# Kernel tuning notes

Measured on AMD Instinct MI355X. Metric: run time of the kernel, lower is better.

## Reference

```python
import jax, jax.numpy as jnp
import numpy as np

R = 40000      # aug_num_rels
E = 500000     # number of relation-graph triplets
DIN = 64       # rel_emb_dim
DH = 64        # hid_dim_rel
H = 8          # num_head
DHID = DH // H # 8
NBIN = 10
L = 2          # num_layer_rel


def _leaky(x):
    return jax.nn.leaky_relu(x, negative_slope=0.2)


def _rel_layer(emb_rel, head, tail, binidx, pw, pb, abin, avec, aw, ab):
    # emb_rel: [R, DH]; head/tail/binidx: [E]
    concat = jnp.concatenate([emb_rel[head], emb_rel[tail]], axis=-1)  # [E, 2*DH]
    z = _leaky(concat @ pw + pb).reshape(-1, H, DHID)                   # [E, H, DHID]
    # attention logits: per-head dot with attn_vec + leaky(bin bias)
    raw = (z * avec[None]).sum(-1) + _leaky(abin[binidx, :, 0])         # [E, H]
    # segmented softmax over edges grouped by head index
    m = jax.ops.segment_max(raw, head, num_segments=R)                  # [R, H]
    e = jnp.exp(raw - m[head])                                          # [E, H]
    s = jax.ops.segment_sum(e, head, num_segments=R)                    # [R, H]
    beta = e / (s[head] + 1e-16)                                        # [E, H]
    msg = (emb_rel[tail] @ aw + ab).reshape(-1, H, DHID) * beta[..., None]
    out = jax.ops.segment_sum(msg, head, num_segments=R)                # [R, H, DHID]
    return out.reshape(R, DH)


def setup_inputs() -> dict:
    key = jax.random.key(0)
    ks = jax.random.split(key, 12)
    ht = jax.random.randint(ks[0], (E, 2), 0, R)
    b = jax.random.randint(ks[1], (E, 1), 0, NBIN)
    relation_triplets = jnp.concatenate([ht, b], axis=-1).astype(jnp.int64)
    sc = 0.05
    return {
        "relation_triplets": relation_triplets,
        "rel_emb_w": jax.random.normal(ks[2], (R, DIN), jnp.float32) * sc,
        "proj1_w": jax.random.normal(ks[3], (DIN, DH), jnp.float32) * sc,
        "proj1_b": jnp.zeros((DH,), jnp.float32),
        "attn_proj_w": jax.random.normal(ks[4], (L, 2 * DH, DH), jnp.float32) * sc,
        "attn_proj_b": jnp.zeros((L, DH), jnp.float32),
        "attn_bin": jax.random.normal(ks[5], (L, NBIN, H, 1), jnp.float32) * sc,
        "attn_vec": jax.random.normal(ks[6], (L, H, DHID), jnp.float32) * sc,
        "aggr_w": jax.random.normal(ks[7], (L, DH, DH), jnp.float32) * sc,
        "aggr_b": jnp.zeros((L, DH), jnp.float32),
        "res_w": jax.random.normal(ks[8], (L, DH, DH), jnp.float32) * sc,
        "res_b": jnp.zeros((L, DH), jnp.float32),
    }


def reference(relation_triplets, rel_emb_w, proj1_w, proj1_b, attn_proj_w,
              attn_proj_b, attn_bin, attn_vec, aggr_w, aggr_b, res_w, res_b):
    head = relation_triplets[:, 0]
    tail = relation_triplets[:, 1]
    binidx = relation_triplets[:, 2]
    emb_rel = jax.nn.relu(rel_emb_w @ proj1_w + proj1_b)  # [R, DH]
    for l in range(L):
        h = _rel_layer(emb_rel, head, tail, binidx,
                       attn_proj_w[l], attn_proj_b[l], attn_bin[l],
                       attn_vec[l], aggr_w[l], aggr_b[l])
        h = jax.nn.relu(h)
        emb_rel = h + jax.nn.relu(emb_rel @ res_w[l] + res_b[l])
    return emb_rel
```

## Files before the change

kernel.cpp:

```cpp
#include <hip/hip_runtime.h>
#include <hip/hip_bf16.h>

typedef __hip_bfloat16 bf16;

#define R_NUM 40000
#define E_NUM 500000

#define W_P1W 0
#define W_P1B 4096
#define W_APW 4160
#define W_APB 20544
#define W_ABIN 20672
#define W_AVEC 20832
#define W_AW 20960
#define W_AB 29152
#define W_RW 29280
#define W_RB 37472
#define W_END 37600
#define WCONV_BLOCKS 147

#define O_FLAG 0
#define O_WBUF 256
#define O_ROWP 150784
#define O_CNTS 310784
#define O_TMP 470784
#define O_PART 634624
#define O_STB 635136
#define O_BIG 2635392
#define XMP_BYTES 10240000ull
#define HR_BYTES 20480000ull
#define XM32_BYTES 20480000ull
#define NEED_LEAN (O_BIG + XMP_BYTES + HR_BYTES)
#define NEED_XM1 (O_BIG + XM32_BYTES)

static __device__ __forceinline__ float b2f(bf16 x) { return __bfloat162float(x); }
static __device__ __forceinline__ float ldv(const float* p, size_t i) { return p[i]; }
static __device__ __forceinline__ float ldv(const bf16* p, size_t i) { return __bfloat162float(p[i]); }
static __device__ __forceinline__ void stv(float* p, size_t i, float v) { p[i] = v; }
static __device__ __forceinline__ void stv(bf16* p, size_t i, float v) { p[i] = __float2bfloat16(v); }

static __device__ __forceinline__ unsigned int f2bb(float x) {
  union { float f; unsigned int u; } v;
  v.f = x;
  unsigned int r = v.u + 0x7FFFu + ((v.u >> 16) & 1u);
  return r >> 16;
}
static __device__ __forceinline__ unsigned int packxm(float xt, float mt) {
  return f2bb(xt) | (f2bb(mt) << 16);
}


__global__ void k_detect_init(const unsigned int* __restrict__ trip_w,
                              const unsigned short* __restrict__ emb_w, int* __restrict__ flag,
                              int* __restrict__ counts, int* __restrict__ stb) {
  int tid = threadIdx.x;
  if (blockIdx.x == 0) {
    if (tid < 64) {
      int lane = tid;
      unsigned int acc = 0;
      for (int i = lane; i < 1024; i += 64) acc |= trip_w[2 * i + 1];
      int votes = 0;
      for (int i = lane; i < 2048; i += 64) {
        unsigned short u = emb_w[2 * i];
        int ex = (u >> 7) & 0xFF;
        if (ex >= 90 && ex <= 130) votes++;
      }
      for (int off = 1; off < 64; off <<= 1) {
        acc |= __shfl_xor(acc, off);
        votes += __shfl_xor(votes, off);
      }
      if (lane == 0) {
        flag[0] = (acc == 0) ? 1 : 0;
        flag[1] = (votes < 1024) ? 1 : 0;
      }
    }
    return;
  }
  int g = (blockIdx.x - 1) * 256 + tid;
  for (int i = g; i < R_NUM; i += 159 * 256) counts[i] = 0;
  if (blockIdx.x == 1 && tid < 64) stb[E_NUM + tid] = 0;
}


static __device__ __forceinline__ void load_edge(const unsigned int* __restrict__ w, int e,
                                                 int i64, int& h, int& t, int& b) {
  if (i64) {
    h = (int)w[6 * e + 0];
    t = (int)w[6 * e + 2];
    b = (int)w[6 * e + 4];
  } else {
    h = (int)w[3 * e + 0];
    t = (int)w[3 * e + 1];
    b = (int)w[3 * e + 2];
  }
}

__global__ void k_hist_wconv(const unsigned int* __restrict__ trip_w, const int* __restrict__ flag,
                             int* __restrict__ counts, const void* p1w, const void* p1b,
                             const void* apw, const void* apb, const void* abin, const void* avec,
                             const void* aw, const void* ab, const void* rw, const void* rb,
                             float* __restrict__ wbuf) {
  if (blockIdx.x < WCONV_BLOCKS) {
    int i = blockIdx.x * 256 + threadIdx.x;
    if (i >= W_END) return;
    const void* src;
    int off;
    if (i < W_P1B) { src = p1w; off = i - W_P1W; }
    else if (i < W_APW) { src = p1b; off = i - W_P1B; }
    else if (i < W_APB) { src = apw; off = i - W_APW; }
    else if (i < W_ABIN) { src = apb; off = i - W_APB; }
    else if (i < W_AVEC) { src = abin; off = i - W_ABIN; }
    else if (i < W_AW) { src = avec; off = i - W_AVEC; }
    else if (i < W_AB) { src = aw; off = i - W_AW; }
    else if (i < W_RW) { src = ab; off = i - W_AB; }
    else if (i < W_RB) { src = rw; off = i - W_RW; }
    else { src = rb; off = i - W_RB; }
    wbuf[i] = flag[1] ? ((const float*)src)[off] : b2f(((const bf16*)src)[off]);
    return;
  }
  int e = (blockIdx.x - WCONV_BLOCKS) * 256 + threadIdx.x;
  if (e >= E_NUM) return;
  int h, t, b;
  load_edge(trip_w, e, flag[0], h, t, b);
  atomicAdd(&counts[h], 1);
}


__global__ void k_scan_a(const int* __restrict__ counts, int* __restrict__ tmp,
                         int* __restrict__ partial) {
  __shared__ int sd[1024];
  int tid = threadIdx.x;
  int idx = blockIdx.x * 1024 + tid;
  int v = (idx < R_NUM) ? counts[idx] : 0;
  sd[tid] = v;
  __syncthreads();
  for (int off = 1; off < 1024; off <<= 1) {
    int t = (tid >= off) ? sd[tid - off] : 0;
    __syncthreads();
    sd[tid] += t;
    __syncthreads();
  }
  if (idx < R_NUM) tmp[idx] = sd[tid];
  if (tid == 1023) partial[blockIdx.x] = sd[1023];
}

__global__ void k_scan_c(const int* __restrict__ counts, const int* __restrict__ tmp,
                         const int* __restrict__ partial, int* __restrict__ row_ptr) {
  __shared__ int soff;
  if (threadIdx.x < 64) {
    int lane = threadIdx.x;
    int p = (lane < (int)blockIdx.x) ? partial[lane] : 0;
    for (int d = 1; d < 64; d <<= 1) p += __shfl_xor(p, d);
    if (lane == 0) soff = p;
  }
  __syncthreads();
  int idx = blockIdx.x * 1024 + threadIdx.x;
  if (idx < R_NUM) row_ptr[idx] = tmp[idx] - counts[idx] + soff;
}

__global__ void k_scatter(const unsigned int* __restrict__ trip_w, const int* __restrict__ flag,
                          int* __restrict__ row_ptr, int* __restrict__ stb) {
  int e = blockIdx.x * 256 + threadIdx.x;
  if (e >= E_NUM) return;
  int h, t, b;
  load_edge(trip_w, e, flag[0], h, t, b);
  int pos = atomicAdd(&row_ptr[h], 1);
  stb[pos] = (t & 0xFFFF) | (b << 16);
}


__global__ void __launch_bounds__(256, 4) k_emb0xm_p(const void* __restrict__ A,
                                                     const int* __restrict__ flag,
                                                     const float* __restrict__ wbuf,
                                                     float* __restrict__ emb,
                                                     unsigned int* __restrict__ XMp,
                                                     float2* __restrict__ HR) {
  int j = threadIdx.x & 63;
  int g = threadIdx.x >> 6;
  int r0 = blockIdx.x * 32 + g * 8;
  int f32 = flag[1];
  __shared__ float sA[32][64];
  for (int k = threadIdx.x; k < 2048; k += 256) {
    int rr = k >> 6, cc = k & 63;
    size_t idx = (size_t)(blockIdx.x * 32 + rr) * 64 + cc;
    sA[rr][cc] = f32 ? ((const float*)A)[idx] : b2f(((const bf16*)A)[idx]);
  }
  __syncthreads();
  int base = g * 8;
  float a[8] = {0.f, 0.f, 0.f, 0.f, 0.f, 0.f, 0.f, 0.f};
  {
    const float* W = wbuf + W_P1W;
    for (int i4 = 0; i4 < 64; i4 += 4) {
      float4 ev[8];
#pragma unroll
      for (int n = 0; n < 8; n++) ev[n] = *(const float4*)&sA[base + n][i4];
#pragma unroll
      for (int di = 0; di < 4; di++) {
        float w = W[(i4 + di) * 64 + j];
#pragma unroll
        for (int n = 0; n < 8; n++)
          a[n] = fmaf(((const float*)&ev[n])[di], w, a[n]);
      }
    }
    float bj = wbuf[W_P1B + j];
#pragma unroll
    for (int n = 0; n < 8; n++) {
      a[n] = fmaxf(a[n] + bj, 0.f);
      emb[(size_t)(r0 + n) * 64 + j] = a[n];
    }
  }
  __syncthreads();
#pragma unroll
  for (int n = 0; n < 8; n++) sA[base + n][j] = a[n];
  __syncthreads();
  {
    const float* pwb = wbuf + W_APW + 4096;
    const float* aw = wbuf + W_AW;
    const float* pwt = wbuf + W_APW;
    const float* rw = wbuf + W_RW;
    float axt[8] = {0.f, 0.f, 0.f, 0.f, 0.f, 0.f, 0.f, 0.f};
    float amt[8] = {0.f, 0.f, 0.f, 0.f, 0.f, 0.f, 0.f, 0.f};
    float axh[8] = {0.f, 0.f, 0.f, 0.f, 0.f, 0.f, 0.f, 0.f};
    float ars[8] = {0.f, 0.f, 0.f, 0.f, 0.f, 0.f, 0.f, 0.f};
    for (int i4 = 0; i4 < 64; i4 += 4) {
      float4 ev[8];
#pragma unroll
      for (int n = 0; n < 8; n++) ev[n] = *(const float4*)&sA[base + n][i4];
#pragma unroll
      for (int di = 0; di < 4; di++) {
        int i = i4 + di;
        float wt = pwb[i * 64 + j];
        float wm = aw[i * 64 + j];
        float wh = pwt[i * 64 + j];
        float wr = rw[i * 64 + j];
#pragma unroll
        for (int n = 0; n < 8; n++) {
          float e = ((const float*)&ev[n])[di];
          axt[n] = fmaf(e, wt, axt[n]);
          amt[n] = fmaf(e, wm, amt[n]);
          axh[n] = fmaf(e, wh, axh[n]);
          ars[n] = fmaf(e, wr, ars[n]);
        }
      }
    }
    float abj = wbuf[W_AB + j];
    float pbj = wbuf[W_APB + j];
    float rbj = wbuf[W_RB + j];
#pragma unroll
    for (int n = 0; n < 8; n++) {
      XMp[(size_t)(r0 + n) * 64 + j] = packxm(axt[n], amt[n] + abj);
      HR[(size_t)(r0 + n) * 64 + j] = make_float2(axh[n] + pbj, fmaxf(ars[n] + rbj, 0.f));
    }
  }
}


__global__ void __launch_bounds__(256, 4) k_xmhr_p(const float* __restrict__ emb,
                                                   const float* __restrict__ wbuf, int l,
                                                   unsigned int* __restrict__ XMp,
                                                   float2* __restrict__ HR) {
  int j = threadIdx.x & 63;
  int g = threadIdx.x >> 6;
  int r0 = blockIdx.x * 32 + g * 8;
  __shared__ float sE[32][64];
  for (int k = threadIdx.x; k < 2048; k += 256) {
    int rr = k >> 6, cc = k & 63;
    sE[rr][cc] = emb[(size_t)(blockIdx.x * 32 + rr) * 64 + cc];
  }
  __syncthreads();
  int base = g * 8;
  const float* pwb = wbuf + W_APW + l * 8192 + 4096;
  const float* aw = wbuf + W_AW + l * 4096;
  const float* pwt = wbuf + W_APW + l * 8192;
  const float* rw = wbuf + W_RW + l * 4096;
  float axt[8] = {0.f, 0.f, 0.f, 0.f, 0.f, 0.f, 0.f, 0.f};
  float amt[8] = {0.f, 0.f, 0.f, 0.f, 0.f, 0.f, 0.f, 0.f};
  float axh[8] = {0.f, 0.f, 0.f, 0.f, 0.f, 0.f, 0.f, 0.f};
  float ars[8] = {0.f, 0.f, 0.f, 0.f, 0.f, 0.f, 0.f, 0.f};
  for (int i4 = 0; i4 < 64; i4 += 4) {
    float4 ev[8];
#pragma unroll
    for (int n = 0; n < 8; n++) ev[n] = *(const float4*)&sE[base + n][i4];
#pragma unroll
    for (int di = 0; di < 4; di++) {
      int i = i4 + di;
      float wt = pwb[i * 64 + j];
      float wm = aw[i * 64 + j];
      float wh = pwt[i * 64 + j];
      float wr = rw[i * 64 + j];
#pragma unroll
      for (int n = 0; n < 8; n++) {
        float e = ((const float*)&ev[n])[di];
        axt[n] = fmaf(e, wt, axt[n]);
        amt[n] = fmaf(e, wm, amt[n]);
        axh[n] = fmaf(e, wh, axh[n]);
        ars[n] = fmaf(e, wr, ars[n]);
      }
    }
  }
  float abj = wbuf[W_AB + l * 64 + j];
  float pbj = wbuf[W_APB + l * 64 + j];
  float rbj = wbuf[W_RB + l * 64 + j];
#pragma unroll
  for (int n = 0; n < 8; n++) {
    XMp[(size_t)(r0 + n) * 64 + j] = packxm(axt[n], amt[n] + abj);
    HR[(size_t)(r0 + n) * 64 + j] = make_float2(axh[n] + pbj, fmaxf(ars[n] + rbj, 0.f));
  }
}


__global__ void __launch_bounds__(256, 4) k_edge_lean(
    const int* __restrict__ row_ptr, const int* __restrict__ stb,
    const unsigned int* __restrict__ XMp, const float2* __restrict__ HR,
    const float* __restrict__ wbuf, int l, float* __restrict__ emb) {
  __shared__ float sab[80];
  int tid = threadIdx.x;
  int lane = tid & 63;
  int w = tid >> 6;
  int hh = lane >> 3;
  if (tid < 80) {
    float a = wbuf[W_ABIN + l * 80 + tid];
    sab[tid] = (a > 0.f) ? a : 0.2f * a;
  }
  __syncthreads();
  float av = wbuf[W_AVEC + l * 64 + lane];

  int r = blockIdx.x * 4 + w;
  float2 hr = HR[(size_t)r * 64 + lane];
  int beg = (r == 0) ? 0 : row_ptr[r - 1];
  int end = row_ptr[r];
  beg = __builtin_amdgcn_readfirstlane(beg);
  end = __builtin_amdgcn_readfirstlane(end);

  float xh = hr.x;
  float num = 0.f, den = 0.f;
  for (int j = beg; j < end; j += 16) {
    int pk[16];
    unsigned int xp[16];
#pragma unroll
    for (int k = 0; k < 16; k++) pk[k] = stb[j + k];
#pragma unroll
    for (int k = 0; k < 16; k++)
      xp[k] = XMp[(size_t)(pk[k] & 0xFFFF) * 64 + lane];
#pragma unroll
    for (int k = 0; k < 16; k++) {
      float xt = __uint_as_float(xp[k] << 16);
      float mt = __uint_as_float(xp[k] & 0xFFFF0000u);
      float z = xh + xt;
      z = (z > 0.f) ? z : 0.2f * z;
      float v = z * av;
      v += __shfl_xor(v, 1);
      v += __shfl_xor(v, 2);
      v += __shfl_xor(v, 4);
      float e = __expf(v + sab[(pk[k] >> 16) * 8 + hh]);
      e = (j + k < end) ? e : 0.f;
      den += e;
      num = fmaf(mt, e, num);
    }
  }
  emb[(size_t)r * 64 + lane] = fmaxf(num / (den + 1e-16f), 0.f) + hr.y;
}


__global__ void k_emb0(const void* __restrict__ A, const int* __restrict__ flag,
                       const float* __restrict__ wbuf, float* __restrict__ emb) {
  int j = threadIdx.x & 63;
  int g = threadIdx.x >> 6;
  int r0 = blockIdx.x * 16 + g * 4;
  int f32 = flag[1];
  __shared__ float sA[16][64];
  for (int k = threadIdx.x; k < 1024; k += 256) {
    int rr = k >> 6, cc = k & 63;
    size_t idx = (size_t)(blockIdx.x * 16 + rr) * 64 + cc;
    sA[rr][cc] = f32 ? ((const float*)A)[idx] : b2f(((const bf16*)A)[idx]);
  }
  __syncthreads();
  const float* W = wbuf + W_P1W;
  float a[4] = {0.f, 0.f, 0.f, 0.f};
  int base = g * 4;
  for (int i = 0; i < 64; i++) {
    float w = W[i * 64 + j];
#pragma unroll
    for (int n = 0; n < 4; n++) a[n] = fmaf(sA[base + n][i], w, a[n]);
  }
  float bj = wbuf[W_P1B + j];
#pragma unroll
  for (int n = 0; n < 4; n++)
    emb[(size_t)(r0 + n) * 64 + j] = fmaxf(a[n] + bj, 0.f);
}

__global__ void k_xm(const float* __restrict__ emb, const float* __restrict__ wbuf, int l,
                     float2* __restrict__ XM) {
  int j = threadIdx.x & 63;
  int g = threadIdx.x >> 6;
  int r0 = blockIdx.x * 16 + g * 4;
  __shared__ float sE[16][64];
  for (int k = threadIdx.x; k < 1024; k += 256) {
    int rr = k >> 6, cc = k & 63;
    sE[rr][cc] = emb[(size_t)(blockIdx.x * 16 + rr) * 64 + cc];
  }
  __syncthreads();
  const float* pwb = wbuf + W_APW + l * 8192 + 4096;
  const float* aw = wbuf + W_AW + l * 4096;
  float axt[4] = {0.f, 0.f, 0.f, 0.f};
  float amt[4] = {0.f, 0.f, 0.f, 0.f};
  int base = g * 4;
  for (int i = 0; i < 64; i++) {
    float wt = pwb[i * 64 + j];
    float wm = aw[i * 64 + j];
#pragma unroll
    for (int n = 0; n < 4; n++) {
      float e = sE[base + n][i];
      axt[n] = fmaf(e, wt, axt[n]);
      amt[n] = fmaf(e, wm, amt[n]);
    }
  }
  float abj = wbuf[W_AB + l * 64 + j];
#pragma unroll
  for (int n = 0; n < 4; n++)
    XM[(size_t)(r0 + n) * 64 + j] = make_float2(axt[n], amt[n] + abj);
}

__global__ void __launch_bounds__(256, 4) k_edge_f(
    const int* __restrict__ row_ptr, const int* __restrict__ stb, const float2* __restrict__ XM,
    const float* __restrict__ wbuf, int l, float* __restrict__ emb) {
  __shared__ float sab[80];
  int tid = threadIdx.x;
  int lane = tid & 63;
  int w = tid >> 6;
  int hh = lane >> 3;
  if (tid < 80) {
    float a = wbuf[W_ABIN + l * 80 + tid];
    sab[tid] = (a > 0.f) ? a : 0.2f * a;
  }
  __syncthreads();

  const float* pwt = wbuf + W_APW + l * 8192;
  const float* rwp = wbuf + W_RW + l * 4096;
  float av = wbuf[W_AVEC + l * 64 + lane];
  float xh0 = wbuf[W_APB + l * 64 + lane];
  float res0 = wbuf[W_RB + l * 64 + lane];

  int r0 = blockIdx.x * 16 + w * 4;
  for (int rr = 0; rr < 4; rr++) {
    int r = r0 + rr;
    float ev = emb[(size_t)r * 64 + lane];
    float xh = xh0, res = res0;
#pragma unroll 16
    for (int i = 0; i < 64; i++) {
      float e = __shfl(ev, i);
      xh = fmaf(e, pwt[i * 64 + lane], xh);
      res = fmaf(e, rwp[i * 64 + lane], res);
    }
    res = fmaxf(res, 0.f);

    int beg = (r == 0) ? 0 : row_ptr[r - 1];
    int end = row_ptr[r];
    beg = __builtin_amdgcn_readfirstlane(beg);
    end = __builtin_amdgcn_readfirstlane(end);

    float num = 0.f, den = 0.f;
    for (int j = beg; j < end; j += 16) {
      int pk[16];
      float2 xmv[16];
#pragma unroll
      for (int k = 0; k < 16; k++) pk[k] = stb[j + k];
#pragma unroll
      for (int k = 0; k < 16; k++) xmv[k] = XM[(size_t)(pk[k] & 0xFFFF) * 64 + lane];
#pragma unroll
      for (int k = 0; k < 16; k++) {
        float z = xh + xmv[k].x;
        z = (z > 0.f) ? z : 0.2f * z;
        float v = z * av;
        v += __shfl_xor(v, 1);
        v += __shfl_xor(v, 2);
        v += __shfl_xor(v, 4);
        float e = __expf(v + sab[(pk[k] >> 16) * 8 + hh]);
        e = (j + k < end) ? e : 0.f;
        den += e;
        num = fmaf(xmv[k].y, e, num);
      }
    }
    emb[(size_t)r * 64 + lane] = fmaxf(num / (den + 1e-16f), 0.f) + res;
  }
}


static __device__ __forceinline__ float dotcol(const float* __restrict__ Wm, float val, int lane) {
  float acc = 0.f;
  for (int i = 0; i < 64; i++) acc = fmaf(__shfl(val, i), Wm[i * 64 + lane], acc);
  return acc;
}

template <typename TIN, typename TOUT>
__global__ void k_edge_d(const int* __restrict__ row_ptr, const int* __restrict__ stb,
                         const float* __restrict__ wbuf, int l, const TIN* __restrict__ emb_in,
                         TOUT* __restrict__ emb_out) {
  __shared__ float sab[80];
  int tid = threadIdx.x;
  int lane = tid & 63;
  int w = tid >> 6;
  int r = blockIdx.x * 4 + w;
  int hh = lane >> 3;
  if (tid < 80) {
    float a = wbuf[W_ABIN + l * 80 + tid];
    sab[tid] = (a > 0.f) ? a : 0.2f * a;
  }
  __syncthreads();
  const float* pwt = wbuf + W_APW + l * 8192;
  const float* pwb = pwt + 4096;
  const float* aw = wbuf + W_AW + l * 4096;
  const float* rw = wbuf + W_RW + l * 4096;

  float ev = ldv(emb_in, (size_t)r * 64 + lane);
  float xh = wbuf[W_APB + l * 64 + lane];
  float res = wbuf[W_RB + l * 64 + lane];
  for (int i = 0; i < 64; i++) {
    float e = __shfl(ev, i);
    xh = fmaf(e, pwt[i * 64 + lane], xh);
    res = fmaf(e, rw[i * 64 + lane], res);
  }
  res = fmaxf(res, 0.f);
  float av = wbuf[W_AVEC + l * 64 + lane];
  float abl = wbuf[W_AB + l * 64 + lane];

  int beg = (r == 0) ? 0 : row_ptr[r - 1];
  int end = row_ptr[r];
  float num = 0.f, den = 0.f;
  for (int j = beg; j < end; j++) {
    int p = stb[j];
    int t = p & 0xFFFF;
    float tv = ldv(emb_in, (size_t)t * 64 + lane);
    float z = xh + dotcol(pwb, tv, lane);
    z = (z > 0.f) ? z : 0.2f * z;
    float v = z * av;
    v += __shfl_xor(v, 1);
    v += __shfl_xor(v, 2);
    v += __shfl_xor(v, 4);
    float e = __expf(v + sab[(p >> 16) * 8 + hh]);
    den += e;
    float mt = dotcol(aw, tv, lane) + abl;
    num = fmaf(mt, e, num);
  }
  stv(emb_out, (size_t)r * 64 + lane, fmaxf(num / (den + 1e-16f), 0.f) + res);
}


extern "C" void kernel_launch(void* const* d_in, const int* in_sizes, int n_in,
                              void* d_out, int out_size, void* d_ws, size_t ws_size,
                              hipStream_t stream) {
  const unsigned int* trip_w = (const unsigned int*)d_in[0];
  const void* rel_emb = d_in[1];
  float* emb = (float*)d_out;

  char* ws = (char*)d_ws;
  int* flag = (int*)(ws + O_FLAG);
  float* wbuf = (float*)(ws + O_WBUF);
  int* row_ptr = (int*)(ws + O_ROWP);
  int* counts = (int*)(ws + O_CNTS);
  int* tmp = (int*)(ws + O_TMP);
  int* partial = (int*)(ws + O_PART);
  int* stb = (int*)(ws + O_STB);
  char* big = ws + O_BIG;

  k_detect_init<<<160, 256, 0, stream>>>(trip_w, (const unsigned short*)rel_emb, flag, counts,
                                         stb);
  int eb_blocks = (E_NUM + 255) / 256;
  k_hist_wconv<<<WCONV_BLOCKS + eb_blocks, 256, 0, stream>>>(
      trip_w, flag, counts, d_in[2], d_in[3], d_in[4], d_in[5], d_in[6], d_in[7], d_in[8],
      d_in[9], d_in[10], d_in[11], wbuf);
  k_scan_a<<<40, 1024, 0, stream>>>(counts, tmp, partial);
  k_scan_c<<<40, 1024, 0, stream>>>(counts, tmp, partial, row_ptr);
  k_scatter<<<eb_blocks, 256, 0, stream>>>(trip_w, flag, row_ptr, stb);

  if (ws_size >= NEED_LEAN) {
    unsigned int* XMp = (unsigned int*)big;
    float2* HR = (float2*)(big + XMP_BYTES);
    k_emb0xm_p<<<R_NUM / 32, 256, 0, stream>>>(rel_emb, flag, wbuf, emb, XMp, HR);
    k_edge_lean<<<R_NUM / 4, 256, 0, stream>>>(row_ptr, stb, XMp, HR, wbuf, 0, emb);
    k_xmhr_p<<<R_NUM / 32, 256, 0, stream>>>(emb, wbuf, 1, XMp, HR);
    k_edge_lean<<<R_NUM / 4, 256, 0, stream>>>(row_ptr, stb, XMp, HR, wbuf, 1, emb);
  } else if (ws_size >= NEED_XM1) {
    float2* XM = (float2*)big;
    k_emb0<<<R_NUM / 16, 256, 0, stream>>>(rel_emb, flag, wbuf, emb);
    k_xm<<<R_NUM / 16, 256, 0, stream>>>(emb, wbuf, 0, XM);
    k_edge_f<<<R_NUM / 16, 256, 0, stream>>>(row_ptr, stb, XM, wbuf, 0, emb);
    k_xm<<<R_NUM / 16, 256, 0, stream>>>(emb, wbuf, 1, XM);
    k_edge_f<<<R_NUM / 16, 256, 0, stream>>>(row_ptr, stb, XM, wbuf, 1, emb);
  } else {
    k_emb0<<<R_NUM / 16, 256, 0, stream>>>(rel_emb, flag, wbuf, emb);
    bf16* embB = (bf16*)big;
    k_edge_d<float, bf16><<<R_NUM / 4, 256, 0, stream>>>(row_ptr, stb, wbuf, 0, emb, embB);
    k_edge_d<bf16, float><<<R_NUM / 4, 256, 0, stream>>>(row_ptr, stb, wbuf, 1, embB, emb);
  }
}
```

Before: 258.4 us.

## Fuse histogram with layer-0 transforms and layer-1 transforms into edge kernel

Result: slower. 267.5 us (+3.5%).

```diff
diff --git a/kernel.cpp b/kernel.cpp
--- a/kernel.cpp
+++ b/kernel.cpp
@@ -5,6 +5,17 @@
 
 #define R_NUM 40000
 #define E_NUM 500000
+#define HIST_BLOCKS 1954
+#define XF_BLOCKS 1250
+
+#define N_CNTS 0
+#define N_ROWP 160000
+#define N_STB 320000
+#define N_XMP0 2320384
+#define N_HR0 12560384
+#define N_XMP1 33040384
+#define N_HR1 43280384
+#define NEED2 63760384ull
 
 #define W_P1W 0
 #define W_P1B 4096
@@ -27,11 +38,6 @@
 #define O_PART 634624
 #define O_STB 635136
 #define O_BIG 2635392
-#define XMP_BYTES 10240000ull
-#define HR_BYTES 20480000ull
-#define XM32_BYTES 20480000ull
-#define NEED_LEAN (O_BIG + XMP_BYTES + HR_BYTES)
-#define NEED_XM1 (O_BIG + XM32_BYTES)
 
 static __device__ __forceinline__ float b2f(bf16 x) { return __bfloat162float(x); }
 static __device__ __forceinline__ float ldv(const float* p, size_t i) { return p[i]; }
@@ -47,6 +53,19 @@
 }
 static __device__ __forceinline__ unsigned int packxm(float xt, float mt) {
   return f2bb(xt) | (f2bb(mt) << 16);
+}
+
+static __device__ __forceinline__ void load_edge(const unsigned int* __restrict__ w, int e,
+                                                 int i64, int& h, int& t, int& b) {
+  if (i64) {
+    h = (int)w[6 * e + 0];
+    t = (int)w[6 * e + 2];
+    b = (int)w[6 * e + 4];
+  } else {
+    h = (int)w[3 * e + 0];
+    t = (int)w[3 * e + 1];
+    b = (int)w[3 * e + 2];
+  }
 }
 
 
@@ -82,18 +101,316 @@
 }
 
 
-static __device__ __forceinline__ void load_edge(const unsigned int* __restrict__ w, int e,
-                                                 int i64, int& h, int& t, int& b) {
-  if (i64) {
-    h = (int)w[6 * e + 0];
-    t = (int)w[6 * e + 2];
-    b = (int)w[6 * e + 4];
-  } else {
-    h = (int)w[3 * e + 0];
-    t = (int)w[3 * e + 1];
-    b = (int)w[3 * e + 2];
-  }
-}
+template <typename WT>
+static __device__ __forceinline__ void xf4t(const float (*sA)[64], int base, int j, int l,
+                                            const WT* __restrict__ apw, const WT* __restrict__ apb,
+                                            const WT* __restrict__ aw, const WT* __restrict__ ab,
+                                            const WT* __restrict__ rw, const WT* __restrict__ rb,
+                                            int r0, unsigned int* __restrict__ XMp,
+                                            float2* __restrict__ HR) {
+  const WT* pwt = apw + l * 8192;
+  const WT* pwb = pwt + 4096;
+  const WT* awl = aw + l * 4096;
+  const WT* rwl = rw + l * 4096;
+  float axt[8] = {0.f, 0.f, 0.f, 0.f, 0.f, 0.f, 0.f, 0.f};
+  float amt[8] = {0.f, 0.f, 0.f, 0.f, 0.f, 0.f, 0.f, 0.f};
+  float axh[8] = {0.f, 0.f, 0.f, 0.f, 0.f, 0.f, 0.f, 0.f};
+  float ars[8] = {0.f, 0.f, 0.f, 0.f, 0.f, 0.f, 0.f, 0.f};
+  for (int i4 = 0; i4 < 64; i4 += 4) {
+    float4 ev[8];
+#pragma unroll
+    for (int n = 0; n < 8; n++) ev[n] = *(const float4*)&sA[base + n][i4];
+#pragma unroll
+    for (int di = 0; di < 4; di++) {
+      int i = i4 + di;
+      float wt = ldv(pwb, (size_t)i * 64 + j);
+      float wm = ldv(awl, (size_t)i * 64 + j);
+      float wh = ldv(pwt, (size_t)i * 64 + j);
+      float wr = ldv(rwl, (size_t)i * 64 + j);
+#pragma unroll
+      for (int n = 0; n < 8; n++) {
+        float e = ((const float*)&ev[n])[di];
+        axt[n] = fmaf(e, wt, axt[n]);
+        amt[n] = fmaf(e, wm, amt[n]);
+        axh[n] = fmaf(e, wh, axh[n]);
+        ars[n] = fmaf(e, wr, ars[n]);
+      }
+    }
+  }
+  float abj = ldv(ab, (size_t)l * 64 + j);
+  float pbj = ldv(apb, (size_t)l * 64 + j);
+  float rbj = ldv(rb, (size_t)l * 64 + j);
+#pragma unroll
+  for (int n = 0; n < 8; n++) {
+    XMp[(size_t)(r0 + n) * 64 + j] = packxm(axt[n], amt[n] + abj);
+    HR[(size_t)(r0 + n) * 64 + j] = make_float2(axh[n] + pbj, fmaxf(ars[n] + rbj, 0.f));
+  }
+}
+
+
+template <typename T>
+static __device__ __forceinline__ void kA_xform(const T* __restrict__ A, const T* __restrict__ p1w,
+                                                const T* __restrict__ p1b,
+                                                const T* __restrict__ apw,
+                                                const T* __restrict__ apb, const T* __restrict__ aw,
+                                                const T* __restrict__ ab, const T* __restrict__ rw,
+                                                const T* __restrict__ rb, int u,
+                                                unsigned int* __restrict__ XMp0,
+                                                float2* __restrict__ HR0, float (*sA)[64]) {
+  int tid = threadIdx.x;
+  int j = tid & 63;
+  int g = tid >> 6;
+  int base = g * 8;
+  for (int k = tid; k < 2048; k += 256) {
+    int rr = k >> 6, cc = k & 63;
+    sA[rr][cc] = ldv(A, (size_t)(u * 32 + rr) * 64 + cc);
+  }
+  __syncthreads();
+  float a[8] = {0.f, 0.f, 0.f, 0.f, 0.f, 0.f, 0.f, 0.f};
+  for (int i4 = 0; i4 < 64; i4 += 4) {
+    float4 ev[8];
+#pragma unroll
+    for (int n = 0; n < 8; n++) ev[n] = *(const float4*)&sA[base + n][i4];
+#pragma unroll
+    for (int di = 0; di < 4; di++) {
+      float w = ldv(p1w, (size_t)(i4 + di) * 64 + j);
+#pragma unroll
+      for (int n = 0; n < 8; n++) a[n] = fmaf(((const float*)&ev[n])[di], w, a[n]);
+    }
+  }
+  float bj = ldv(p1b, j);
+#pragma unroll
+  for (int n = 0; n < 8; n++) a[n] = fmaxf(a[n] + bj, 0.f);
+  __syncthreads();
+#pragma unroll
+  for (int n = 0; n < 8; n++) sA[base + n][j] = a[n];
+  __syncthreads();
+  xf4t<T>((const float(*)[64])sA, base, j, 0, apw, apb, aw, ab, rw, rb, u * 32 + base, XMp0, HR0);
+}
+
+__global__ void __launch_bounds__(256, 4) kA(const unsigned int* __restrict__ trip_w,
+                                             const int* __restrict__ flag,
+                                             const void* __restrict__ A, const void* p1w,
+                                             const void* p1b, const void* apw, const void* apb,
+                                             const void* aw, const void* ab, const void* rw,
+                                             const void* rb, int* __restrict__ counts,
+                                             unsigned int* __restrict__ XMp0,
+                                             float2* __restrict__ HR0) {
+  if (blockIdx.x < HIST_BLOCKS) {
+    int e = blockIdx.x * 256 + threadIdx.x;
+    if (e < E_NUM) {
+      int h = flag[0] ? (int)trip_w[6 * e] : (int)trip_w[3 * e];
+      atomicAdd(&counts[h], 1);
+    }
+    return;
+  }
+  __shared__ float sA[32][64];
+  int u = blockIdx.x - HIST_BLOCKS;
+  if (flag[1])
+    kA_xform<float>((const float*)A, (const float*)p1w, (const float*)p1b, (const float*)apw,
+                    (const float*)apb, (const float*)aw, (const float*)ab, (const float*)rw,
+                    (const float*)rb, u, XMp0, HR0, sA);
+  else
+    kA_xform<bf16>((const bf16*)A, (const bf16*)p1w, (const bf16*)p1b, (const bf16*)apw,
+                   (const bf16*)apb, (const bf16*)aw, (const bf16*)ab, (const bf16*)rw,
+                   (const bf16*)rb, u, XMp0, HR0, sA);
+}
+
+
+__global__ void __launch_bounds__(1024) k_scan1(const int* __restrict__ counts,
+                                                int* __restrict__ row_ptr) {
+  __shared__ int sp[1024];
+  int tid = threadIdx.x;
+  int base = tid * 40;
+  int local[40];
+  int s = 0;
+  if (base < R_NUM) {
+#pragma unroll
+    for (int k = 0; k < 40; k++) {
+      int v = counts[base + k];
+      local[k] = s;
+      s += v;
+    }
+  }
+  sp[tid] = s;
+  __syncthreads();
+  for (int off = 1; off < 1024; off <<= 1) {
+    int t = (tid >= off) ? sp[tid - off] : 0;
+    __syncthreads();
+    sp[tid] += t;
+    __syncthreads();
+  }
+  int pre = (tid == 0) ? 0 : sp[tid - 1];
+  if (base < R_NUM) {
+#pragma unroll
+    for (int k = 0; k < 40; k++) row_ptr[base + k] = pre + local[k];
+  }
+}
+
+__global__ void k_scatter(const unsigned int* __restrict__ trip_w, const int* __restrict__ flag,
+                          int* __restrict__ row_ptr, int* __restrict__ stb) {
+  int e = blockIdx.x * 256 + threadIdx.x;
+  if (e >= E_NUM) return;
+  int h, t, b;
+  load_edge(trip_w, e, flag[0], h, t, b);
+  int pos = atomicAdd(&row_ptr[h], 1);
+  stb[pos] = (t & 0xFFFF) | (b << 16);
+}
+
+
+template <typename T>
+static __device__ __forceinline__ void kB_body(const int* __restrict__ row_ptr,
+                                               const int* __restrict__ stb,
+                                               const unsigned int* __restrict__ XMp0,
+                                               const float2* __restrict__ HR0,
+                                               const T* __restrict__ apw, const T* __restrict__ apb,
+                                               const T* __restrict__ abin,
+                                               const T* __restrict__ avec, const T* __restrict__ aw,
+                                               const T* __restrict__ ab, const T* __restrict__ rw,
+                                               const T* __restrict__ rb,
+                                               unsigned int* __restrict__ XMp1,
+                                               float2* __restrict__ HR1, float (*sE)[64],
+                                               float* sab) {
+  int tid = threadIdx.x;
+  int lane = tid & 63;
+  int w = tid >> 6;
+  int hh = lane >> 3;
+  if (tid < 80) {
+    float a = ldv(abin, tid);
+    sab[tid] = (a > 0.f) ? a : 0.2f * a;
+  }
+  __syncthreads();
+  float av = ldv(avec, lane);
+  int rbase = blockIdx.x * 32 + w * 8;
+#pragma unroll 1
+  for (int n = 0; n < 8; n++) {
+    int r = rbase + n;
+    float2 hr = HR0[(size_t)r * 64 + lane];
+    int beg = (r == 0) ? 0 : row_ptr[r - 1];
+    int end = row_ptr[r];
+    beg = __builtin_amdgcn_readfirstlane(beg);
+    end = __builtin_amdgcn_readfirstlane(end);
+    float xh = hr.x;
+    float num = 0.f, den = 0.f;
+    for (int jj = beg; jj < end; jj += 16) {
+      int pk[16];
+      unsigned int xp[16];
+#pragma unroll
+      for (int k = 0; k < 16; k++) pk[k] = stb[jj + k];
+#pragma unroll
+      for (int k = 0; k < 16; k++) xp[k] = XMp0[(size_t)(pk[k] & 0xFFFF) * 64 + lane];
+#pragma unroll
+      for (int k = 0; k < 16; k++) {
+        float xt = __uint_as_float(xp[k] << 16);
+        float mt = __uint_as_float(xp[k] & 0xFFFF0000u);
+        float z = xh + xt;
+        z = (z > 0.f) ? z : 0.2f * z;
+        float v = z * av;
+        v += __shfl_xor(v, 1);
+        v += __shfl_xor(v, 2);
+        v += __shfl_xor(v, 4);
+        float e = __expf(v + sab[(pk[k] >> 16) * 8 + hh]);
+        e = (jj + k < end) ? e : 0.f;
+        den += e;
+        num = fmaf(mt, e, num);
+      }
+    }
+    sE[w * 8 + n][lane] = fmaxf(num / (den + 1e-16f), 0.f) + hr.y;
+  }
+  __syncthreads();
+  xf4t<T>((const float(*)[64])sE, w * 8, lane, 1, apw, apb, aw, ab, rw, rb,
+          blockIdx.x * 32 + w * 8, XMp1, HR1);
+}
+
+__global__ void __launch_bounds__(256, 4) kB(const int* __restrict__ row_ptr,
+                                             const int* __restrict__ stb,
+                                             const int* __restrict__ flag,
+                                             const unsigned int* __restrict__ XMp0,
+                                             const float2* __restrict__ HR0, const void* apw,
+                                             const void* apb, const void* abin, const void* avec,
+                                             const void* aw, const void* ab, const void* rw,
+                                             const void* rb, unsigned int* __restrict__ XMp1,
+                                             float2* __restrict__ HR1) {
+  __shared__ float sE[32][64];
+  __shared__ float sab[80];
+  if (flag[1])
+    kB_body<float>(row_ptr, stb, XMp0, HR0, (const float*)apw, (const float*)apb,
+                   (const float*)abin, (const float*)avec, (const float*)aw, (const float*)ab,
+                   (const float*)rw, (const float*)rb, XMp1, HR1, sE, sab);
+  else
+    kB_body<bf16>(row_ptr, stb, XMp0, HR0, (const bf16*)apw, (const bf16*)apb, (const bf16*)abin,
+                  (const bf16*)avec, (const bf16*)aw, (const bf16*)ab, (const bf16*)rw,
+                  (const bf16*)rb, XMp1, HR1, sE, sab);
+}
+
+
+template <typename T>
+static __device__ __forceinline__ void kC_body(const int* __restrict__ row_ptr,
+                                               const int* __restrict__ stb,
+                                               const unsigned int* __restrict__ XMp1,
+                                               const float2* __restrict__ HR1,
+                                               const T* __restrict__ abin,
+                                               const T* __restrict__ avec,
+                                               float* __restrict__ out, float* sab) {
+  int tid = threadIdx.x;
+  int lane = tid & 63;
+  int w = tid >> 6;
+  int hh = lane >> 3;
+  if (tid < 80) {
+    float a = ldv(abin, 80 + tid);
+    sab[tid] = (a > 0.f) ? a : 0.2f * a;
+  }
+  __syncthreads();
+  float av = ldv(avec, 64 + lane);
+
+  int r = blockIdx.x * 4 + w;
+  float2 hr = HR1[(size_t)r * 64 + lane];
+  int beg = (r == 0) ? 0 : row_ptr[r - 1];
+  int end = row_ptr[r];
+  beg = __builtin_amdgcn_readfirstlane(beg);
+  end = __builtin_amdgcn_readfirstlane(end);
+
+  float xh = hr.x;
+  float num = 0.f, den = 0.f;
+  for (int j = beg; j < end; j += 16) {
+    int pk[16];
+    unsigned int xp[16];
+#pragma unroll
+    for (int k = 0; k < 16; k++) pk[k] = stb[j + k];
+#pragma unroll
+    for (int k = 0; k < 16; k++) xp[k] = XMp1[(size_t)(pk[k] & 0xFFFF) * 64 + lane];
+#pragma unroll
+    for (int k = 0; k < 16; k++) {
+      float xt = __uint_as_float(xp[k] << 16);
+      float mt = __uint_as_float(xp[k] & 0xFFFF0000u);
+      float z = xh + xt;
+      z = (z > 0.f) ? z : 0.2f * z;
+      float v = z * av;
+      v += __shfl_xor(v, 1);
+      v += __shfl_xor(v, 2);
+      v += __shfl_xor(v, 4);
+      float e = __expf(v + sab[(pk[k] >> 16) * 8 + hh]);
+      e = (j + k < end) ? e : 0.f;
+      den += e;
+      num = fmaf(mt, e, num);
+    }
+  }
+  out[(size_t)r * 64 + lane] = fmaxf(num / (den + 1e-16f), 0.f) + hr.y;
+}
+
+__global__ void __launch_bounds__(256, 4) kC(const int* __restrict__ row_ptr,
+                                             const int* __restrict__ stb,
+                                             const int* __restrict__ flag,
+                                             const unsigned int* __restrict__ XMp1,
+                                             const float2* __restrict__ HR1, const void* abin,
+                                             const void* avec, float* __restrict__ out) {
+  __shared__ float sab[80];
+  if (flag[1])
+    kC_body<float>(row_ptr, stb, XMp1, HR1, (const float*)abin, (const float*)avec, out, sab);
+  else
+    kC_body<bf16>(row_ptr, stb, XMp1, HR1, (const bf16*)abin, (const bf16*)avec, out, sab);
+}
+
 
 __global__ void k_hist_wconv(const unsigned int* __restrict__ trip_w, const int* __restrict__ flag,
                              int* __restrict__ counts, const void* p1w, const void* p1b,
@@ -125,243 +442,6 @@
   atomicAdd(&counts[h], 1);
 }
 
-
-__global__ void k_scan_a(const int* __restrict__ counts, int* __restrict__ tmp,
-                         int* __restrict__ partial) {
-  __shared__ int sd[1024];
-  int tid = threadIdx.x;
-  int idx = blockIdx.x * 1024 + tid;
-  int v = (idx < R_NUM) ? counts[idx] : 0;
-  sd[tid] = v;
-  __syncthreads();
-  for (int off = 1; off < 1024; off <<= 1) {
-    int t = (tid >= off) ? sd[tid - off] : 0;
-    __syncthreads();
-    sd[tid] += t;
-    __syncthreads();
-  }
-  if (idx < R_NUM) tmp[idx] = sd[tid];
-  if (tid == 1023) partial[blockIdx.x] = sd[1023];
-}
-
-__global__ void k_scan_c(const int* __restrict__ counts, const int* __restrict__ tmp,
-                         const int* __restrict__ partial, int* __restrict__ row_ptr) {
-  __shared__ int soff;
-  if (threadIdx.x < 64) {
-    int lane = threadIdx.x;
-    int p = (lane < (int)blockIdx.x) ? partial[lane] : 0;
-    for (int d = 1; d < 64; d <<= 1) p += __shfl_xor(p, d);
-    if (lane == 0) soff = p;
-  }
-  __syncthreads();
-  int idx = blockIdx.x * 1024 + threadIdx.x;
-  if (idx < R_NUM) row_ptr[idx] = tmp[idx] - counts[idx] + soff;
-}
-
-__global__ void k_scatter(const unsigned int* __restrict__ trip_w, const int* __restrict__ flag,
-                          int* __restrict__ row_ptr, int* __restrict__ stb) {
-  int e = blockIdx.x * 256 + threadIdx.x;
-  if (e >= E_NUM) return;
-  int h, t, b;
-  load_edge(trip_w, e, flag[0], h, t, b);
-  int pos = atomicAdd(&row_ptr[h], 1);
-  stb[pos] = (t & 0xFFFF) | (b << 16);
-}
-
-
-__global__ void __launch_bounds__(256, 4) k_emb0xm_p(const void* __restrict__ A,
-                                                     const int* __restrict__ flag,
-                                                     const float* __restrict__ wbuf,
-                                                     float* __restrict__ emb,
-                                                     unsigned int* __restrict__ XMp,
-                                                     float2* __restrict__ HR) {
-  int j = threadIdx.x & 63;
-  int g = threadIdx.x >> 6;
-  int r0 = blockIdx.x * 32 + g * 8;
-  int f32 = flag[1];
-  __shared__ float sA[32][64];
-  for (int k = threadIdx.x; k < 2048; k += 256) {
-    int rr = k >> 6, cc = k & 63;
-    size_t idx = (size_t)(blockIdx.x * 32 + rr) * 64 + cc;
-    sA[rr][cc] = f32 ? ((const float*)A)[idx] : b2f(((const bf16*)A)[idx]);
-  }
-  __syncthreads();
-  int base = g * 8;
-  float a[8] = {0.f, 0.f, 0.f, 0.f, 0.f, 0.f, 0.f, 0.f};
-  {
-    const float* W = wbuf + W_P1W;
-    for (int i4 = 0; i4 < 64; i4 += 4) {
-      float4 ev[8];
-#pragma unroll
-      for (int n = 0; n < 8; n++) ev[n] = *(const float4*)&sA[base + n][i4];
-#pragma unroll
-      for (int di = 0; di < 4; di++) {
-        float w = W[(i4 + di) * 64 + j];
-#pragma unroll
-        for (int n = 0; n < 8; n++)
-          a[n] = fmaf(((const float*)&ev[n])[di], w, a[n]);
-      }
-    }
-    float bj = wbuf[W_P1B + j];
-#pragma unroll
-    for (int n = 0; n < 8; n++) {
-      a[n] = fmaxf(a[n] + bj, 0.f);
-      emb[(size_t)(r0 + n) * 64 + j] = a[n];
-    }
-  }
-  __syncthreads();
-#pragma unroll
-  for (int n = 0; n < 8; n++) sA[base + n][j] = a[n];
-  __syncthreads();
-  {
-    const float* pwb = wbuf + W_APW + 4096;
-    const float* aw = wbuf + W_AW;
-    const float* pwt = wbuf + W_APW;
-    const float* rw = wbuf + W_RW;
-    float axt[8] = {0.f, 0.f, 0.f, 0.f, 0.f, 0.f, 0.f, 0.f};
-    float amt[8] = {0.f, 0.f, 0.f, 0.f, 0.f, 0.f, 0.f, 0.f};
-    float axh[8] = {0.f, 0.f, 0.f, 0.f, 0.f, 0.f, 0.f, 0.f};
-    float ars[8] = {0.f, 0.f, 0.f, 0.f, 0.f, 0.f, 0.f, 0.f};
-    for (int i4 = 0; i4 < 64; i4 += 4) {
-      float4 ev[8];
-#pragma unroll
-      for (int n = 0; n < 8; n++) ev[n] = *(const float4*)&sA[base + n][i4];
-#pragma unroll
-      for (int di = 0; di < 4; di++) {
-        int i = i4 + di;
-        float wt = pwb[i * 64 + j];
-        float wm = aw[i * 64 + j];
-        float wh = pwt[i * 64 + j];
-        float wr = rw[i * 64 + j];
-#pragma unroll
-        for (int n = 0; n < 8; n++) {
-          float e = ((const float*)&ev[n])[di];
-          axt[n] = fmaf(e, wt, axt[n]);
-          amt[n] = fmaf(e, wm, amt[n]);
-          axh[n] = fmaf(e, wh, axh[n]);
-          ars[n] = fmaf(e, wr, ars[n]);
-        }
-      }
-    }
-    float abj = wbuf[W_AB + j];
-    float pbj = wbuf[W_APB + j];
-    float rbj = wbuf[W_RB + j];
-#pragma unroll
-    for (int n = 0; n < 8; n++) {
-      XMp[(size_t)(r0 + n) * 64 + j] = packxm(axt[n], amt[n] + abj);
-      HR[(size_t)(r0 + n) * 64 + j] = make_float2(axh[n] + pbj, fmaxf(ars[n] + rbj, 0.f));
-    }
-  }
-}
-
-
-__global__ void __launch_bounds__(256, 4) k_xmhr_p(const float* __restrict__ emb,
-                                                   const float* __restrict__ wbuf, int l,
-                                                   unsigned int* __restrict__ XMp,
-                                                   float2* __restrict__ HR) {
-  int j = threadIdx.x & 63;
-  int g = threadIdx.x >> 6;
-  int r0 = blockIdx.x * 32 + g * 8;
-  __shared__ float sE[32][64];
-  for (int k = threadIdx.x; k < 2048; k += 256) {
-    int rr = k >> 6, cc = k & 63;
-    sE[rr][cc] = emb[(size_t)(blockIdx.x * 32 + rr) * 64 + cc];
-  }
-  __syncthreads();
-  int base = g * 8;
-  const float* pwb = wbuf + W_APW + l * 8192 + 4096;
-  const float* aw = wbuf + W_AW + l * 4096;
-  const float* pwt = wbuf + W_APW + l * 8192;
-  const float* rw = wbuf + W_RW + l * 4096;
-  float axt[8] = {0.f, 0.f, 0.f, 0.f, 0.f, 0.f, 0.f, 0.f};
-  float amt[8] = {0.f, 0.f, 0.f, 0.f, 0.f, 0.f, 0.f, 0.f};
-  float axh[8] = {0.f, 0.f, 0.f, 0.f, 0.f, 0.f, 0.f, 0.f};
-  float ars[8] = {0.f, 0.f, 0.f, 0.f, 0.f, 0.f, 0.f, 0.f};
-  for (int i4 = 0; i4 < 64; i4 += 4) {
-    float4 ev[8];
-#pragma unroll
-    for (int n = 0; n < 8; n++) ev[n] = *(const float4*)&sE[base + n][i4];
-#pragma unroll
-    for (int di = 0; di < 4; di++) {
-      int i = i4 + di;
-      float wt = pwb[i * 64 + j];
-      float wm = aw[i * 64 + j];
-      float wh = pwt[i * 64 + j];
-      float wr = rw[i * 64 + j];
-#pragma unroll
-      for (int n = 0; n < 8; n++) {
-        float e = ((const float*)&ev[n])[di];
-        axt[n] = fmaf(e, wt, axt[n]);
-        amt[n] = fmaf(e, wm, amt[n]);
-        axh[n] = fmaf(e, wh, axh[n]);
-        ars[n] = fmaf(e, wr, ars[n]);
-      }
-    }
-  }
-  float abj = wbuf[W_AB + l * 64 + j];
-  float pbj = wbuf[W_APB + l * 64 + j];
-  float rbj = wbuf[W_RB + l * 64 + j];
-#pragma unroll
-  for (int n = 0; n < 8; n++) {
-    XMp[(size_t)(r0 + n) * 64 + j] = packxm(axt[n], amt[n] + abj);
-    HR[(size_t)(r0 + n) * 64 + j] = make_float2(axh[n] + pbj, fmaxf(ars[n] + rbj, 0.f));
-  }
-}
-
-
-__global__ void __launch_bounds__(256, 4) k_edge_lean(
-    const int* __restrict__ row_ptr, const int* __restrict__ stb,
-    const unsigned int* __restrict__ XMp, const float2* __restrict__ HR,
-    const float* __restrict__ wbuf, int l, float* __restrict__ emb) {
-  __shared__ float sab[80];
-  int tid = threadIdx.x;
-  int lane = tid & 63;
-  int w = tid >> 6;
-  int hh = lane >> 3;
-  if (tid < 80) {
-    float a = wbuf[W_ABIN + l * 80 + tid];
-    sab[tid] = (a > 0.f) ? a : 0.2f * a;
-  }
-  __syncthreads();
-  float av = wbuf[W_AVEC + l * 64 + lane];
-
-  int r = blockIdx.x * 4 + w;
-  float2 hr = HR[(size_t)r * 64 + lane];
-  int beg = (r == 0) ? 0 : row_ptr[r - 1];
-  int end = row_ptr[r];
-  beg = __builtin_amdgcn_readfirstlane(beg);
-  end = __builtin_amdgcn_readfirstlane(end);
-
-  float xh = hr.x;
-  float num = 0.f, den = 0.f;
-  for (int j = beg; j < end; j += 16) {
-    int pk[16];
-    unsigned int xp[16];
-#pragma unroll
-    for (int k = 0; k < 16; k++) pk[k] = stb[j + k];
-#pragma unroll
-    for (int k = 0; k < 16; k++)
-      xp[k] = XMp[(size_t)(pk[k] & 0xFFFF) * 64 + lane];
-#pragma unroll
-    for (int k = 0; k < 16; k++) {
-      float xt = __uint_as_float(xp[k] << 16);
-      float mt = __uint_as_float(xp[k] & 0xFFFF0000u);
-      float z = xh + xt;
-      z = (z > 0.f) ? z : 0.2f * z;
-      float v = z * av;
-      v += __shfl_xor(v, 1);
-      v += __shfl_xor(v, 2);
-      v += __shfl_xor(v, 4);
-      float e = __expf(v + sab[(pk[k] >> 16) * 8 + hh]);
-      e = (j + k < end) ? e : 0.f;
-      den += e;
-      num = fmaf(mt, e, num);
-    }
-  }
-  emb[(size_t)r * 64 + lane] = fmaxf(num / (den + 1e-16f), 0.f) + hr.y;
-}
-
-
 __global__ void k_emb0(const void* __restrict__ A, const int* __restrict__ flag,
                        const float* __restrict__ wbuf, float* __restrict__ emb) {
   int j = threadIdx.x & 63;
@@ -388,103 +468,6 @@
   for (int n = 0; n < 4; n++)
     emb[(size_t)(r0 + n) * 64 + j] = fmaxf(a[n] + bj, 0.f);
 }
-
-__global__ void k_xm(const float* __restrict__ emb, const float* __restrict__ wbuf, int l,
-                     float2* __restrict__ XM) {
-  int j = threadIdx.x & 63;
-  int g = threadIdx.x >> 6;
-  int r0 = blockIdx.x * 16 + g * 4;
-  __shared__ float sE[16][64];
-  for (int k = threadIdx.x; k < 1024; k += 256) {
-    int rr = k >> 6, cc = k & 63;
-    sE[rr][cc] = emb[(size_t)(blockIdx.x * 16 + rr) * 64 + cc];
-  }
-  __syncthreads();
-  const float* pwb = wbuf + W_APW + l * 8192 + 4096;
-  const float* aw = wbuf + W_AW + l * 4096;
-  float axt[4] = {0.f, 0.f, 0.f, 0.f};
-  float amt[4] = {0.f, 0.f, 0.f, 0.f};
-  int base = g * 4;
-  for (int i = 0; i < 64; i++) {
-    float wt = pwb[i * 64 + j];
-    float wm = aw[i * 64 + j];
-#pragma unroll
-    for (int n = 0; n < 4; n++) {
-      float e = sE[base + n][i];
-      axt[n] = fmaf(e, wt, axt[n]);
-      amt[n] = fmaf(e, wm, amt[n]);
-    }
-  }
-  float abj = wbuf[W_AB + l * 64 + j];
-#pragma unroll
-  for (int n = 0; n < 4; n++)
-    XM[(size_t)(r0 + n) * 64 + j] = make_float2(axt[n], amt[n] + abj);
-}
-
-__global__ void __launch_bounds__(256, 4) k_edge_f(
-    const int* __restrict__ row_ptr, const int* __restrict__ stb, const float2* __restrict__ XM,
-    const float* __restrict__ wbuf, int l, float* __restrict__ emb) {
-  __shared__ float sab[80];
-  int tid = threadIdx.x;
-  int lane = tid & 63;
-  int w = tid >> 6;
-  int hh = lane >> 3;
-  if (tid < 80) {
-    float a = wbuf[W_ABIN + l * 80 + tid];
-    sab[tid] = (a > 0.f) ? a : 0.2f * a;
-  }
-  __syncthreads();
-
-  const float* pwt = wbuf + W_APW + l * 8192;
-  const float* rwp = wbuf + W_RW + l * 4096;
-  float av = wbuf[W_AVEC + l * 64 + lane];
-  float xh0 = wbuf[W_APB + l * 64 + lane];
-  float res0 = wbuf[W_RB + l * 64 + lane];
-
-  int r0 = blockIdx.x * 16 + w * 4;
-  for (int rr = 0; rr < 4; rr++) {
-    int r = r0 + rr;
-    float ev = emb[(size_t)r * 64 + lane];
-    float xh = xh0, res = res0;
-#pragma unroll 16
-    for (int i = 0; i < 64; i++) {
-      float e = __shfl(ev, i);
-      xh = fmaf(e, pwt[i * 64 + lane], xh);
-      res = fmaf(e, rwp[i * 64 + lane], res);
-    }
-    res = fmaxf(res, 0.f);
-
-    int beg = (r == 0) ? 0 : row_ptr[r - 1];
-    int end = row_ptr[r];
-    beg = __builtin_amdgcn_readfirstlane(beg);
-    end = __builtin_amdgcn_readfirstlane(end);
-
-    float num = 0.f, den = 0.f;
-    for (int j = beg; j < end; j += 16) {
-      int pk[16];
-      float2 xmv[16];
-#pragma unroll
-      for (int k = 0; k < 16; k++) pk[k] = stb[j + k];
-#pragma unroll
-      for (int k = 0; k < 16; k++) xmv[k] = XM[(size_t)(pk[k] & 0xFFFF) * 64 + lane];
-#pragma unroll
-      for (int k = 0; k < 16; k++) {
-        float z = xh + xmv[k].x;
-        z = (z > 0.f) ? z : 0.2f * z;
-        float v = z * av;
-        v += __shfl_xor(v, 1);
-        v += __shfl_xor(v, 2);
-        v += __shfl_xor(v, 4);
-        float e = __expf(v + sab[(pk[k] >> 16) * 8 + hh]);
-        e = (j + k < end) ? e : 0.f;
-        den += e;
-        num = fmaf(xmv[k].y, e, num);
-      }
-    }
-    emb[(size_t)r * 64 + lane] = fmaxf(num / (den + 1e-16f), 0.f) + res;
-  }
-}
-
 
 static __device__ __forceinline__ float dotcol(const float* __restrict__ Wm, float val, int lane) {
   float acc = 0.f;
@@ -552,42 +535,46 @@
   const unsigned int* trip_w = (const unsigned int*)d_in[0];
   const void* rel_emb = d_in[1];
   float* emb = (float*)d_out;
-
   char* ws = (char*)d_ws;
-  int* flag = (int*)(ws + O_FLAG);
-  float* wbuf = (float*)(ws + O_WBUF);
-  int* row_ptr = (int*)(ws + O_ROWP);
-  int* counts = (int*)(ws + O_CNTS);
-  int* tmp = (int*)(ws + O_TMP);
-  int* partial = (int*)(ws + O_PART);
-  int* stb = (int*)(ws + O_STB);
-  char* big = ws + O_BIG;
-
-  k_detect_init<<<160, 256, 0, stream>>>(trip_w, (const unsigned short*)rel_emb, flag, counts,
-                                         stb);
-  int eb_blocks = (E_NUM + 255) / 256;
-  k_hist_wconv<<<WCONV_BLOCKS + eb_blocks, 256, 0, stream>>>(
-      trip_w, flag, counts, d_in[2], d_in[3], d_in[4], d_in[5], d_in[6], d_in[7], d_in[8],
-      d_in[9], d_in[10], d_in[11], wbuf);
-  k_scan_a<<<40, 1024, 0, stream>>>(counts, tmp, partial);
-  k_scan_c<<<40, 1024, 0, stream>>>(counts, tmp, partial, row_ptr);
-  k_scatter<<<eb_blocks, 256, 0, stream>>>(trip_w, flag, row_ptr, stb);
-
-  if (ws_size >= NEED_LEAN) {
-    unsigned int* XMp = (unsigned int*)big;
-    float2* HR = (float2*)(big + XMP_BYTES);
-    k_emb0xm_p<<<R_NUM / 32, 256, 0, stream>>>(rel_emb, flag, wbuf, emb, XMp, HR);
-    k_edge_lean<<<R_NUM / 4, 256, 0, stream>>>(row_ptr, stb, XMp, HR, wbuf, 0, emb);
-    k_xmhr_p<<<R_NUM / 32, 256, 0, stream>>>(emb, wbuf, 1, XMp, HR);
-    k_edge_lean<<<R_NUM / 4, 256, 0, stream>>>(row_ptr, stb, XMp, HR, wbuf, 1, emb);
-  } else if (ws_size >= NEED_XM1) {
-    float2* XM = (float2*)big;
-    k_emb0<<<R_NUM / 16, 256, 0, stream>>>(rel_emb, flag, wbuf, emb);
-    k_xm<<<R_NUM / 16, 256, 0, stream>>>(emb, wbuf, 0, XM);
-    k_edge_f<<<R_NUM / 16, 256, 0, stream>>>(row_ptr, stb, XM, wbuf, 0, emb);
-    k_xm<<<R_NUM / 16, 256, 0, stream>>>(emb, wbuf, 1, XM);
-    k_edge_f<<<R_NUM / 16, 256, 0, stream>>>(row_ptr, stb, XM, wbuf, 1, emb);
-  } else {
+
+  if (ws_size >= NEED2) {
+    int* counts = (int*)(ws + N_CNTS);
+    int* row_ptr = (int*)(ws + N_ROWP);
+    int* stb = (int*)(ws + N_STB);
+    unsigned int* XMp0 = (unsigned int*)(ws + N_XMP0);
+    float2* HR0 = (float2*)(ws + N_HR0);
+    unsigned int* XMp1 = (unsigned int*)(ws + N_XMP1);
+    float2* HR1 = (float2*)(ws + N_HR1);
+    int* flag = (int*)(ws + N_STB + (E_NUM + 64) * 4);
+
+    k_detect_init<<<160, 256, 0, stream>>>(trip_w, (const unsigned short*)rel_emb, flag, counts,
+                                           stb);
+    kA<<<HIST_BLOCKS + XF_BLOCKS, 256, 0, stream>>>(trip_w, flag, rel_emb, d_in[2], d_in[3],
+                                                    d_in[4], d_in[5], d_in[8], d_in[9], d_in[10],
+                                                    d_in[11], counts, XMp0, HR0);
+    k_scan1<<<1, 1024, 0, stream>>>(counts, row_ptr);
+    k_scatter<<<HIST_BLOCKS, 256, 0, stream>>>(trip_w, flag, row_ptr, stb);
+    kB<<<XF_BLOCKS, 256, 0, stream>>>(row_ptr, stb, flag, XMp0, HR0, d_in[4], d_in[5], d_in[6],
+                                      d_in[7], d_in[8], d_in[9], d_in[10], d_in[11], XMp1, HR1);
+    kC<<<R_NUM / 4, 256, 0, stream>>>(row_ptr, stb, flag, XMp1, HR1, d_in[6], d_in[7], emb);
+    return;
+  }
+
+  {
+    int* flag = (int*)(ws + O_FLAG);
+    float* wbuf = (float*)(ws + O_WBUF);
+    int* row_ptr = (int*)(ws + O_ROWP);
+    int* counts = (int*)(ws + O_CNTS);
+    int* stb = (int*)(ws + O_STB);
+    char* big = ws + O_BIG;
+
+    k_detect_init<<<160, 256, 0, stream>>>(trip_w, (const unsigned short*)rel_emb, flag, counts,
+                                           stb);
+    k_hist_wconv<<<WCONV_BLOCKS + HIST_BLOCKS, 256, 0, stream>>>(
+        trip_w, flag, counts, d_in[2], d_in[3], d_in[4], d_in[5], d_in[6], d_in[7], d_in[8],
+        d_in[9], d_in[10], d_in[11], wbuf);
+    k_scan1<<<1, 1024, 0, stream>>>(counts, row_ptr);
+    k_scatter<<<HIST_BLOCKS, 256, 0, stream>>>(trip_w, flag, row_ptr, stb);
     k_emb0<<<R_NUM / 16, 256, 0, stream>>>(rel_emb, flag, wbuf, emb);
     bf16* embB = (bf16*)big;
     k_edge_d<float, bf16><<<R_NUM / 4, 256, 0, stream>>>(row_ptr, stb, wbuf, 0, emb, embB);
```
